# Performance work log

Hardware: AMD Instinct MI355X
Metric: run time of the kernel (lower is better)

The kernel has to match this reference:

```python
import jax, jax.numpy as jnp
import numpy as np

N_TRAIN = 8192
B = 4096
D_IN = 4
D_OUT = 3


def setup_inputs() -> dict:
    key = jax.random.key(0)
    k1, k2, k3, k4 = jax.random.split(key, 4)
    x = jax.random.normal(k1, (B, D_IN), dtype=jnp.float32)
    train_X = jax.random.normal(k2, (N_TRAIN, D_IN), dtype=jnp.float32)
    Y = jax.random.normal(k3, (N_TRAIN,), dtype=jnp.float32)
    # fc1 weight, Kaiming-uniform-ish init scale for Linear(4, 3, bias=False)
    W = jax.random.uniform(k4, (D_OUT, D_IN), dtype=jnp.float32, minval=-0.5, maxval=0.5)
    h = jnp.asarray(1.0, dtype=jnp.float32)  # learnable bandwidth parameter
    return {"x": x, "train_X": train_X, "Y": Y, "W": W, "h": h}


def reference(x, train_X, Y, W, h):
    # xw = fc1(x): [B, 3]
    Xw = x @ W.T
    # torch.mv(W, x_j) for all j at once: [N, 3]
    Z = train_X @ W.T
    # leave-one-out Gaussian kernel, applied elementwise per output dim:
    # gauss(u) = exp(-u^2 / 2) with a=1, mu=0, sigma=1
    diff = (Z[:, None, :] - Xw[None, :, :]) / h          # [N, B, 3]
    k = jnp.exp(-0.5 * diff * diff)                      # [N, B, 3]
    numerator = jnp.einsum('nbd,n->bd', k, Y)            # sum_j k_j * Y[j]
    denominator = jnp.sum(k, axis=0)                     # sum_j k_j
    return numerator / denominator                       # [B, 3]
```

## Files before the change

### kernel.cpp

```cpp
#include <hip/hip_runtime.h>
#include <hip/hip_bf16.h>

#if defined(__has_builtin)
#if __has_builtin(__builtin_amdgcn_exp2f)
#define FAST_EXP2(x) __builtin_amdgcn_exp2f(x)
#endif
#endif
#ifndef FAST_EXP2
#define FAST_EXP2(x) exp2f(x)
#endif

#define N_TRAIN 8192
#define BSZ 4096
#define NOUT (BSZ * 3)
#define BLK 256

__global__ __launch_bounds__(BLK) void prep_k(
    const float4* __restrict__ x4,
    const float4* __restrict__ tX4,
    const float*  __restrict__ Y,
    const float*  __restrict__ W,
    const float*  __restrict__ hptr,
    float4* __restrict__ AY,
    float4* __restrict__ B4,
    float4* __restrict__ XW)
{
    int idx = blockIdx.x * BLK + threadIdx.x;
    float h = hptr[0];
    float c = -0.72134752044448170368f / (h * h);

    const float4* Wv = (const float4*)W;
    float4 w0 = Wv[0], w1 = Wv[1], w2 = Wv[2];

    if (idx < N_TRAIN) {
        float4 t = tX4[idx];
        float z0 = t.x * w0.x + t.y * w0.y + t.z * w0.z + t.w * w0.w;
        float z1 = t.x * w1.x + t.y * w1.y + t.z * w1.z + t.w * w1.w;
        float z2 = t.x * w2.x + t.y * w2.y + t.z * w2.z + t.w * w2.w;
        AY[idx] = make_float4(c * z0 * z0, c * z1 * z1, c * z2 * z2, Y[idx]);
        B4[idx] = make_float4(-2.f * c * z0, -2.f * c * z1, -2.f * c * z2, 0.f);
    } else {
        int b = idx - N_TRAIN;
        float4 t = x4[b];
        float x0 = t.x * w0.x + t.y * w0.y + t.z * w0.z + t.w * w0.w;
        float x1 = t.x * w1.x + t.y * w1.y + t.z * w1.z + t.w * w1.w;
        float x2 = t.x * w2.x + t.y * w2.y + t.z * w2.z + t.w * w2.w;
        XW[b] = make_float4(x0, x1, x2, 0.f);
    }
}

__global__ __launch_bounds__(BLK) void kde_k(
    const float4* __restrict__ AY,
    const float4* __restrict__ B4,
    const float4* __restrict__ XW,
    float* __restrict__ NP,
    float* __restrict__ DP,
    int nb)
{
    __shared__ float4 sA[256];
    __shared__ float4 sB[256];

    int tid  = threadIdx.x;
    int bblk = blockIdx.x & 15;
    int seg  = blockIdx.x >> 4;
    int n0   = seg * nb;
    int b    = (bblk << 8) + tid;

    float4 xw = XW[b];
    float num0 = 0.f, num1 = 0.f, num2 = 0.f;
    float den0 = 0.f, den1 = 0.f, den2 = 0.f;

    for (int t0 = 0; t0 < nb; t0 += 256) {
        sA[tid] = AY[n0 + t0 + tid];
        sB[tid] = B4[n0 + t0 + tid];
        __syncthreads();

        #pragma unroll 8
        for (int i = 0; i < 256; ++i) {
            float4 a  = sA[i];
            float4 bb = sB[i];
            float e0 = FAST_EXP2(fmaf(bb.x, xw.x, a.x));
            float e1 = FAST_EXP2(fmaf(bb.y, xw.y, a.y));
            float e2 = FAST_EXP2(fmaf(bb.z, xw.z, a.z));
            den0 += e0;
            den1 += e1;
            den2 += e2;
            num0 = fmaf(e0, a.w, num0);
            num1 = fmaf(e1, a.w, num1);
            num2 = fmaf(e2, a.w, num2);
        }
        __syncthreads();
    }

    int base = seg * NOUT + b * 3;
    NP[base + 0] = num0;
    NP[base + 1] = num1;
    NP[base + 2] = num2;
    DP[base + 0] = den0;
    DP[base + 1] = den1;
    DP[base + 2] = den2;
}

__global__ __launch_bounds__(BLK) void reduce_k(
    const float* __restrict__ NP,
    const float* __restrict__ DP,
    float* __restrict__ out,
    int ns)
{
    int t = blockIdx.x * BLK + threadIdx.x;
    float n = 0.f, d = 0.f;
    for (int s = 0; s < ns; ++s) {
        n += NP[s * NOUT + t];
        d += DP[s * NOUT + t];
    }
    out[t] = n / d;
}

extern "C" void kernel_launch(void* const* d_in, const int* in_sizes, int n_in,
                              void* d_out, int out_size, void* d_ws, size_t ws_size,
                              hipStream_t stream) {
    const float* x   = (const float*)d_in[0];
    const float* tX  = (const float*)d_in[1];
    const float* Y   = (const float*)d_in[2];
    const float* W   = (const float*)d_in[3];
    const float* h   = (const float*)d_in[4];
    float* out = (float*)d_out;

    float4* AY = (float4*)d_ws;
    float4* B4 = AY + N_TRAIN;
    float4* XW = B4 + N_TRAIN;
    float*  NP = (float*)(XW + BSZ);

    size_t fixed_bytes = (size_t)(2 * N_TRAIN + BSZ) * sizeof(float4);
    int ns = 32;
    while (ns > 1 &&
           fixed_bytes + (size_t)ns * NOUT * 2 * sizeof(float) > ws_size) {
        ns >>= 1;
    }
    float* DP = NP + (size_t)ns * NOUT;
    int nb = N_TRAIN / ns;

    prep_k<<<(N_TRAIN + BSZ) / BLK, BLK, 0, stream>>>(
        (const float4*)x, (const float4*)tX, Y, W, h, AY, B4, XW);

    kde_k<<<16 * ns, BLK, 0, stream>>>(AY, B4, XW, NP, DP, nb);

    reduce_k<<<NOUT / BLK, BLK, 0, stream>>>(NP, DP, out, ns);
}
```

Before: 40.09 us.

## Register-block 4 queries per thread and read train data via uniform loads

Each thread now handles four batch rows, reusing every loaded training record across four queries. The shared-memory staging and barriers are removed; all threads in a block read the same interleaved train record directly, which should become scalar or broadcast loads. The partial-sum layout becomes dimension-major for coalesced stores, and the split count rises to 128 segments to keep enough blocks in flight. The cost is more registers per thread and a larger partial buffer for the reduce kernel to read.

```diff
diff --git a/kernel.cpp b/kernel.cpp
--- a/kernel.cpp
+++ b/kernel.cpp
@@ -14,6 +14,9 @@
 #define BSZ 4096
 #define NOUT (BSZ * 3)
 #define BLK 256
+#define RPT 4
+#define BPB (BLK * RPT)
+#define NBB (BSZ / BPB)
 
 __global__ __launch_bounds__(BLK) void prep_k(
     const float4* __restrict__ x4,
@@ -21,8 +24,7 @@
     const float*  __restrict__ Y,
     const float*  __restrict__ W,
     const float*  __restrict__ hptr,
-    float4* __restrict__ AY,
-    float4* __restrict__ B4,
+    float4* __restrict__ TB,
     float4* __restrict__ XW)
 {
     int idx = blockIdx.x * BLK + threadIdx.x;
@@ -37,8 +39,8 @@
         float z0 = t.x * w0.x + t.y * w0.y + t.z * w0.z + t.w * w0.w;
         float z1 = t.x * w1.x + t.y * w1.y + t.z * w1.z + t.w * w1.w;
         float z2 = t.x * w2.x + t.y * w2.y + t.z * w2.z + t.w * w2.w;
-        AY[idx] = make_float4(c * z0 * z0, c * z1 * z1, c * z2 * z2, Y[idx]);
-        B4[idx] = make_float4(-2.f * c * z0, -2.f * c * z1, -2.f * c * z2, 0.f);
+        TB[2 * idx]     = make_float4(c * z0 * z0, c * z1 * z1, c * z2 * z2, Y[idx]);
+        TB[2 * idx + 1] = make_float4(-2.f * c * z0, -2.f * c * z1, -2.f * c * z2, 0.f);
     } else {
         int b = idx - N_TRAIN;
         float4 t = x4[b];
@@ -50,55 +52,58 @@
 }
 
 __global__ __launch_bounds__(BLK) void kde_k(
-    const float4* __restrict__ AY,
-    const float4* __restrict__ B4,
+    const float4* __restrict__ TB,
     const float4* __restrict__ XW,
     float* __restrict__ NP,
     float* __restrict__ DP,
     int nb)
 {
-    __shared__ float4 sA[256];
-    __shared__ float4 sB[256];
+    int tid  = threadIdx.x;
+    int bblk = blockIdx.x & (NBB - 1);
+    int seg  = blockIdx.x / NBB;
+    int n0   = seg * nb;
+    int b0   = bblk * BPB + tid;
 
-    int tid  = threadIdx.x;
-    int bblk = blockIdx.x & 15;
-    int seg  = blockIdx.x >> 4;
-    int n0   = seg * nb;
-    int b    = (bblk << 8) + tid;
+    float4 xw[RPT];
+    #pragma unroll
+    for (int r = 0; r < RPT; ++r) xw[r] = XW[b0 + r * BLK];
 
-    float4 xw = XW[b];
-    float num0 = 0.f, num1 = 0.f, num2 = 0.f;
-    float den0 = 0.f, den1 = 0.f, den2 = 0.f;
+    float num[RPT][3], den[RPT][3];
+    #pragma unroll
+    for (int r = 0; r < RPT; ++r)
+        #pragma unroll
+        for (int d = 0; d < 3; ++d) { num[r][d] = 0.f; den[r][d] = 0.f; }
 
-    for (int t0 = 0; t0 < nb; t0 += 256) {
-        sA[tid] = AY[n0 + t0 + tid];
-        sB[tid] = B4[n0 + t0 + tid];
-        __syncthreads();
+    #pragma unroll 2
+    for (int t = 0; t < nb; ++t) {
+        int n = n0 + t;
+        float4 a  = TB[2 * n];
+        float4 bb = TB[2 * n + 1];
 
-        #pragma unroll 8
-        for (int i = 0; i < 256; ++i) {
-            float4 a  = sA[i];
-            float4 bb = sB[i];
-            float e0 = FAST_EXP2(fmaf(bb.x, xw.x, a.x));
-            float e1 = FAST_EXP2(fmaf(bb.y, xw.y, a.y));
-            float e2 = FAST_EXP2(fmaf(bb.z, xw.z, a.z));
-            den0 += e0;
-            den1 += e1;
-            den2 += e2;
-            num0 = fmaf(e0, a.w, num0);
-            num1 = fmaf(e1, a.w, num1);
-            num2 = fmaf(e2, a.w, num2);
+        #pragma unroll
+        for (int r = 0; r < RPT; ++r) {
+            float e0 = FAST_EXP2(fmaf(bb.x, xw[r].x, a.x));
+            float e1 = FAST_EXP2(fmaf(bb.y, xw[r].y, a.y));
+            float e2 = FAST_EXP2(fmaf(bb.z, xw[r].z, a.z));
+            den[r][0] += e0;
+            den[r][1] += e1;
+            den[r][2] += e2;
+            num[r][0] = fmaf(e0, a.w, num[r][0]);
+            num[r][1] = fmaf(e1, a.w, num[r][1]);
+            num[r][2] = fmaf(e2, a.w, num[r][2]);
         }
-        __syncthreads();
     }
 
-    int base = seg * NOUT + b * 3;
-    NP[base + 0] = num0;
-    NP[base + 1] = num1;
-    NP[base + 2] = num2;
-    DP[base + 0] = den0;
-    DP[base + 1] = den1;
-    DP[base + 2] = den2;
+    size_t sb = (size_t)seg * NOUT;
+    #pragma unroll
+    for (int r = 0; r < RPT; ++r) {
+        int b = b0 + r * BLK;
+        #pragma unroll
+        for (int d = 0; d < 3; ++d) {
+            NP[sb + (size_t)d * BSZ + b] = num[r][d];
+            DP[sb + (size_t)d * BSZ + b] = den[r][d];
+        }
+    }
 }
 
 __global__ __launch_bounds__(BLK) void reduce_k(
@@ -110,10 +115,12 @@
     int t = blockIdx.x * BLK + threadIdx.x;
     float n = 0.f, d = 0.f;
     for (int s = 0; s < ns; ++s) {
-        n += NP[s * NOUT + t];
-        d += DP[s * NOUT + t];
+        n += NP[(size_t)s * NOUT + t];
+        d += DP[(size_t)s * NOUT + t];
     }
-    out[t] = n / d;
+    int b  = t & (BSZ - 1);
+    int dd = t >> 12;
+    out[b * 3 + dd] = n / d;
 }
 
 extern "C" void kernel_launch(void* const* d_in, const int* in_sizes, int n_in,
@@ -126,13 +133,12 @@
     const float* h   = (const float*)d_in[4];
     float* out = (float*)d_out;
 
-    float4* AY = (float4*)d_ws;
-    float4* B4 = AY + N_TRAIN;
-    float4* XW = B4 + N_TRAIN;
+    float4* TB = (float4*)d_ws;
+    float4* XW = TB + 2 * N_TRAIN;
     float*  NP = (float*)(XW + BSZ);
 
     size_t fixed_bytes = (size_t)(2 * N_TRAIN + BSZ) * sizeof(float4);
-    int ns = 32;
+    int ns = 128;
     while (ns > 1 &&
            fixed_bytes + (size_t)ns * NOUT * 2 * sizeof(float) > ws_size) {
         ns >>= 1;
@@ -141,9 +147,9 @@
     int nb = N_TRAIN / ns;
 
     prep_k<<<(N_TRAIN + BSZ) / BLK, BLK, 0, stream>>>(
-        (const float4*)x, (const float4*)tX, Y, W, h, AY, B4, XW);
+        (const float4*)x, (const float4*)tX, Y, W, h, TB, XW);
 
-    kde_k<<<16 * ns, BLK, 0, stream>>>(AY, B4, XW, NP, DP, nb);
+    kde_k<<<NBB * ns, BLK, 0, stream>>>(TB, XW, NP, DP, nb);
 
     reduce_k<<<NOUT / BLK, BLK, 0, stream>>>(NP, DP, out, ns);
 }
```

Result: slower. 72.32 us (+80.4%).
